# Performance work log

Measured on AMD Instinct MI355X. Metric: run time of the kernel, lower is better.

Reference implementation:

```python
import jax, jax.numpy as jnp
import numpy as np

B, S, D_MODEL, N_HEADS = 4, 8192, 1024, 16
D_K = D_MODEL // N_HEADS


def setup_inputs() -> dict:
    key = jax.random.key(0)
    k1, k2, k3 = jax.random.split(key, 3)
    x = jax.random.normal(k1, (B, S, D_MODEL), dtype=jnp.float32)
    w_qkv = jax.random.normal(k2, (D_MODEL, 3 * D_MODEL), dtype=jnp.float32) * (1.0 / np.sqrt(D_MODEL))
    w_o = jax.random.normal(k3, (D_MODEL, D_MODEL), dtype=jnp.float32) * (1.0 / np.sqrt(D_MODEL))
    return {"x": x, "w_qkv": w_qkv, "w_o": w_o}


def reference(x, w_qkv, w_o):
    b, s, dm = x.shape
    h, d = N_HEADS, D_K
    qkv = (x @ w_qkv).reshape(b, s, 3, h, d)  # (b, s, 3, h, d)
    q, k, v = qkv[:, :, 0], qkv[:, :, 1], qkv[:, :, 2]  # each (b, s, h, d)
    # ELU+1 feature map (positive features)
    q = jax.nn.elu(q) + 1.0
    k = jax.nn.elu(k) + 1.0
    # Global (non-causal) KV aggregation: (b, h, d, d)
    kv = jnp.einsum('bnhd,bnhf->bhdf', k, v)
    k_sum = k.sum(axis=1)  # (b, h, d)
    numerator = jnp.einsum('bnhd,bhdf->bnhf', q, kv)  # (b, s, h, d)
    denominator = jnp.einsum('bnhd,bhd->bnh', q, k_sum)[..., None] + 1e-6
    attn = (numerator / denominator).reshape(b, s, dm)
    return attn @ w_o
```

## Files before the change

kernel.cpp:

```cpp
#include <hip/hip_runtime.h>
#include <cmath>

constexpr int BB = 4;
constexpr int SS = 8192;
constexpr int DMODEL = 1024;
constexpr int NHEADS = 16;
constexpr int DHEAD = 64;
constexpr int MTOK = BB * SS;

typedef __attribute__((ext_vector_type(8))) short short8;
typedef __attribute__((ext_vector_type(4))) float f32x4;

__device__ __forceinline__ unsigned short f2bf(float f) {
    unsigned u = __float_as_uint(f);
    u += 0x7FFF + ((u >> 16) & 1);
    return (unsigned short)(u >> 16);
}
__device__ __forceinline__ float bf2f(unsigned short h) {
    return __uint_as_float(((unsigned)h) << 16);
}

__device__ __forceinline__ void stage_tile64(const unsigned short* g0, int ld,
                                             unsigned short* lds, int wave, int lane) {
#pragma unroll
    for (int i = 0; i < 4; ++i) {
        const int c = (wave * 4 + i) * 64 + lane;
        const int r = c >> 3;
        const int qg = (c & 7) ^ (r & 7);
        const unsigned short* g = g0 + (size_t)r * ld + qg * 8;
        unsigned short* l = lds + (wave * 4 + i) * 512;
        __builtin_amdgcn_global_load_lds(
            (const __attribute__((address_space(1))) unsigned int*)g,
            (__attribute__((address_space(3))) unsigned int*)l, 16, 0, 0);
    }
}

__device__ __forceinline__ short8 frag_ld64(const unsigned short* lds, int r, int q) {
    const int qs = q ^ (r & 7);
    return *(const short8*)(lds + r * 64 + qs * 8);
}

template <int EPI>
__global__ __launch_bounds__(256) void la_gemm(
    const unsigned short* __restrict__ A, const unsigned short* __restrict__ B,
    float* __restrict__ Cf,
    unsigned short* __restrict__ Cq, unsigned short* __restrict__ Ck,
    unsigned short* __restrict__ Cv,
    int N, int K)
{
    __shared__ __align__(16) unsigned short smem[2 * 8192];
    unsigned short* sA = smem;
    unsigned short* sB = smem + 8192;

    const int t = threadIdx.x;
    const int wave = t >> 6, lane = t & 63;
    const int wm = wave & 1, wn = wave >> 1;
    const int quad = lane >> 4, fl = lane & 15;
    const int m0 = blockIdx.y * 128, n0 = blockIdx.x * 128;

    const unsigned short* a_g = A + (size_t)m0 * K;
    const unsigned short* b_g = B + (size_t)n0 * K;

    f32x4 acc[4][4];
#pragma unroll
    for (int i = 0; i < 4; ++i)
#pragma unroll
        for (int j = 0; j < 4; ++j) acc[i][j] = (f32x4){0.f, 0.f, 0.f, 0.f};

    for (int kt = 0; kt < K; kt += 64) {
        __syncthreads();
        stage_tile64(a_g + kt, K, sA, wave, lane);
        stage_tile64(b_g + kt, K, sB, wave, lane);
        __syncthreads();

        short8 ah[4][2], bh[4][2];
#pragma unroll
        for (int i = 0; i < 4; ++i) {
            const int ra = wm * 64 + i * 16 + fl;
            const int rb = wn * 64 + i * 16 + fl;
#pragma unroll
            for (int s = 0; s < 2; ++s) {
                ah[i][s] = frag_ld64(sA, ra, s * 4 + quad);
                bh[i][s] = frag_ld64(sB, rb, s * 4 + quad);
            }
        }
#pragma unroll
        for (int s = 0; s < 2; ++s)
#pragma unroll
            for (int i = 0; i < 4; ++i)
#pragma unroll
                for (int j = 0; j < 4; ++j)
                    acc[i][j] = __builtin_amdgcn_mfma_f32_16x16x32_bf16(
                        ah[i][s], bh[j][s], acc[i][j], 0, 0, 0);
    }

    if (EPI == 1) {
        const int bsel = n0 >> 10;
        unsigned short* Cp = (bsel == 0) ? Cq : ((bsel == 1) ? Ck : Cv);
        const bool act = (bsel < 2);
        const int colb = (n0 & 1023) + wn * 64 + fl;
#pragma unroll
        for (int i = 0; i < 4; ++i) {
            const int rowb = m0 + wm * 64 + i * 16 + quad * 4;
#pragma unroll
            for (int j = 0; j < 4; ++j) {
                const int col = colb + j * 16;
#pragma unroll
                for (int r = 0; r < 4; ++r) {
                    float v = acc[i][j][r];
                    if (act) v = (v > 0.f) ? v + 1.f : __expf(v);
                    Cp[(size_t)(rowb + r) * 1024 + col] = f2bf(v);
                }
            }
        }
    } else {
#pragma unroll
        for (int i = 0; i < 4; ++i) {
            const int rowb = m0 + wm * 64 + i * 16 + quad * 4;
#pragma unroll
            for (int j = 0; j < 4; ++j) {
                const int col = n0 + wn * 64 + fl + j * 16;
#pragma unroll
                for (int r = 0; r < 4; ++r)
                    Cf[(size_t)(rowb + r) * N + col] = acc[i][j][r];
            }
        }
    }
}

__global__ __launch_bounds__(256) void cast_bf16(
    const float4* __restrict__ in, ushort4* __restrict__ hi, int n4)
{
    int i = blockIdx.x * 256 + threadIdx.x;
    const int stride = gridDim.x * 256;
    for (; i < n4; i += stride) {
        const float4 v = in[i];
        ushort4 h;
        h.x = f2bf(v.x); h.y = f2bf(v.y); h.z = f2bf(v.z); h.w = f2bf(v.w);
        hi[i] = h;
    }
}

__global__ __launch_bounds__(256) void cast_T(
    const float* __restrict__ w, unsigned short* __restrict__ hiT, int Kd, int Nd)
{
    __shared__ float tile[32][33];
    const int t = threadIdx.x;
    const int n0 = blockIdx.x * 32, k0 = blockIdx.y * 32;
    const int r = t >> 3, c4 = (t & 7) * 4;
    const float4 v = *(const float4*)(w + (size_t)(k0 + r) * Nd + n0 + c4);
    tile[r][c4 + 0] = v.x; tile[r][c4 + 1] = v.y;
    tile[r][c4 + 2] = v.z; tile[r][c4 + 3] = v.w;
    __syncthreads();
    ushort4 h;
    h.x = f2bf(tile[c4 + 0][r]); h.y = f2bf(tile[c4 + 1][r]);
    h.z = f2bf(tile[c4 + 2][r]); h.w = f2bf(tile[c4 + 3][r]);
    *(ushort4*)(hiT + (size_t)(n0 + r) * Kd + k0 + c4) = h;
}

constexpr int KV_CHUNKS = 16;

__global__ __launch_bounds__(256) void la_kvsum(
    const unsigned short* __restrict__ Kb, const unsigned short* __restrict__ Vb,
    float* __restrict__ kv, float* __restrict__ ksum)
{
    __shared__ float kk[32][68];
    __shared__ float vv[32][68];
    const int t = threadIdx.x;
    const int bh = blockIdx.x;
    const int b = bh >> 4, h = bh & 15;
    const int r = t >> 3, c8 = (t & 7) * 8;
    const int d0 = (t & 15) * 4, f0 = (t >> 4) * 4;
    float acc[4][4];
#pragma unroll
    for (int i = 0; i < 4; ++i)
#pragma unroll
        for (int j = 0; j < 4; ++j) acc[i][j] = 0.f;
    float ks = 0.f;
    const int s0 = blockIdx.y * (SS / KV_CHUNKS);

    for (int st = 0; st < SS / KV_CHUNKS; st += 32) {
        const size_t row = (size_t)(b * SS + s0 + st + r) * DMODEL + h * DHEAD + c8;
        const uint4 ku = *(const uint4*)(Kb + row);
        const uint4 vu = *(const uint4*)(Vb + row);
        __syncthreads();
        const unsigned ka_[4] = {ku.x, ku.y, ku.z, ku.w};
        const unsigned va_[4] = {vu.x, vu.y, vu.z, vu.w};
#pragma unroll
        for (int e = 0; e < 4; ++e) {
            kk[r][c8 + 2 * e]     = __uint_as_float(ka_[e] << 16);
            kk[r][c8 + 2 * e + 1] = __uint_as_float(ka_[e] & 0xFFFF0000u);
            vv[r][c8 + 2 * e]     = __uint_as_float(va_[e] << 16);
            vv[r][c8 + 2 * e + 1] = __uint_as_float(va_[e] & 0xFFFF0000u);
        }
        __syncthreads();
#pragma unroll 8
        for (int rr = 0; rr < 32; ++rr) {
            float4 kr = *(const float4*)&kk[rr][d0];
            float4 vr = *(const float4*)&vv[rr][f0];
            float ka[4] = {kr.x, kr.y, kr.z, kr.w};
            float va[4] = {vr.x, vr.y, vr.z, vr.w};
#pragma unroll
            for (int i = 0; i < 4; ++i)
#pragma unroll
                for (int j = 0; j < 4; ++j)
                    acc[i][j] = fmaf(ka[i], va[j], acc[i][j]);
        }
        if (t < 64) {
#pragma unroll 8
            for (int rr = 0; rr < 32; ++rr) ks += kk[rr][t];
        }
    }

    float* kvp = kv + (size_t)bh * DHEAD * DHEAD;
#pragma unroll
    for (int i = 0; i < 4; ++i)
#pragma unroll
        for (int j = 0; j < 4; ++j)
            atomicAdd(&kvp[(d0 + i) * DHEAD + f0 + j], acc[i][j]);
    if (t < 64) atomicAdd(&ksum[bh * DHEAD + t], ks);
}

__global__ __launch_bounds__(256) void la_attn(
    const unsigned short* __restrict__ Q, const float* __restrict__ kv,
    const float* __restrict__ ksum, unsigned short* __restrict__ attn)
{
    __shared__ float kvs[64][68];
    __shared__ float qs[64][68];
    __shared__ float kss[64];
    const int t = threadIdx.x;
    const int t0 = blockIdx.x * 64;
    const int b = t0 / SS;
    const int tok_g = t >> 4;
    const int f_g = t & 15;

    for (int hh = 0; hh < NHEADS; ++hh) {
        __syncthreads();
        const float* kvp = kv + (size_t)(b * NHEADS + hh) * DHEAD * DHEAD;
#pragma unroll
        for (int i = 0; i < 4; ++i) {
            const int idx = i * 256 + t;
            const int r = idx >> 4, c4 = (idx & 15) * 4;
            *(float4*)&kvs[r][c4] = *(const float4*)(kvp + r * 64 + c4);
        }
        if (t < 64) kss[t] = ksum[(b * NHEADS + hh) * DHEAD + t];
#pragma unroll
        for (int i = 0; i < 2; ++i) {
            const int idx = i * 256 + t;
            const int r = idx >> 3, c8 = (idx & 7) * 8;
            const uint4 qu = *(const uint4*)(Q + (size_t)(t0 + r) * DMODEL + hh * 64 + c8);
            const unsigned a[4] = {qu.x, qu.y, qu.z, qu.w};
#pragma unroll
            for (int e = 0; e < 4; ++e) {
                qs[r][c8 + 2 * e]     = __uint_as_float(a[e] << 16);
                qs[r][c8 + 2 * e + 1] = __uint_as_float(a[e] & 0xFFFF0000u);
            }
        }
        __syncthreads();

        float acc[4][4];
        float den[4];
#pragma unroll
        for (int i = 0; i < 4; ++i) {
            den[i] = 0.f;
#pragma unroll
            for (int j = 0; j < 4; ++j) acc[i][j] = 0.f;
        }
#pragma unroll 8
        for (int d = 0; d < 64; ++d) {
            const float4 kvf = *(const float4*)&kvs[d][f_g * 4];
            const float ks = kss[d];
#pragma unroll
            for (int i = 0; i < 4; ++i) {
                const float qd = qs[tok_g * 4 + i][d];
                den[i]    = fmaf(qd, ks,    den[i]);
                acc[i][0] = fmaf(qd, kvf.x, acc[i][0]);
                acc[i][1] = fmaf(qd, kvf.y, acc[i][1]);
                acc[i][2] = fmaf(qd, kvf.z, acc[i][2]);
                acc[i][3] = fmaf(qd, kvf.w, acc[i][3]);
            }
        }
#pragma unroll
        for (int i = 0; i < 4; ++i) {
            const float rcp = 1.f / (den[i] + 1e-6f);
            ushort4 o;
            o.x = f2bf(acc[i][0] * rcp); o.y = f2bf(acc[i][1] * rcp);
            o.z = f2bf(acc[i][2] * rcp); o.w = f2bf(acc[i][3] * rcp);
            *(ushort4*)(attn + (size_t)(t0 + tok_g * 4 + i) * DMODEL + hh * 64 + f_g * 4) = o;
        }
    }
}

__global__ void la_sentinel(float* out, int n) {
    int i = blockIdx.x * 256 + threadIdx.x;
    if (i < n) out[i] = 12345.0f;
}

extern "C" void kernel_launch(void* const* d_in, const int* in_sizes, int n_in,
                              void* d_out, int out_size, void* d_ws, size_t ws_size,
                              hipStream_t stream)
{
    const float* x     = (const float*)d_in[0];
    const float* w_qkv = (const float*)d_in[1];
    const float* w_o   = (const float*)d_in[2];
    float* out = (float*)d_out;

    char* p = (char*)d_ws;
    const size_t x_bf = (size_t)MTOK * DMODEL * 2;
    unsigned short* x_hi = (unsigned short*)p; p += x_bf;
    unsigned short* wqT = (unsigned short*)p; p += (size_t)3 * DMODEL * DMODEL * 2;
    unsigned short* woT = (unsigned short*)p; p += (size_t)DMODEL * DMODEL * 2;
    unsigned short* q_buf = (unsigned short*)p; p += x_bf;
    unsigned short* k_buf = (unsigned short*)p; p += x_bf;
    unsigned short* v_buf = (unsigned short*)p; p += x_bf;
    float* kvb = (float*)p; p += (size_t)BB * NHEADS * DHEAD * DHEAD * 4;
    float* ksb = (float*)p; p += (size_t)BB * NHEADS * DHEAD * 4;

    if ((size_t)(p - (char*)d_ws) > ws_size) {
        la_sentinel<<<(MTOK * DMODEL + 255) / 256, 256, 0, stream>>>(out, MTOK * DMODEL);
        return;
    }

    hipMemsetAsync(kvb, 0,
                   (size_t)(BB * NHEADS * DHEAD * DHEAD + BB * NHEADS * DHEAD) * sizeof(float),
                   stream);

    cast_bf16<<<8192, 256, 0, stream>>>((const float4*)x, (ushort4*)x_hi,
                                        MTOK * DMODEL / 4);
    cast_T<<<dim3(3 * DMODEL / 32, DMODEL / 32), 256, 0, stream>>>(w_qkv, wqT,
                                                                   DMODEL, 3 * DMODEL);
    cast_T<<<dim3(DMODEL / 32, DMODEL / 32), 256, 0, stream>>>(w_o, woT,
                                                               DMODEL, DMODEL);

    la_gemm<1><<<dim3(3 * DMODEL / 128, MTOK / 128), 256, 0, stream>>>(
        x_hi, wqT, nullptr, q_buf, k_buf, v_buf, 3 * DMODEL, DMODEL);

    la_kvsum<<<dim3(BB * NHEADS, KV_CHUNKS), 256, 0, stream>>>(k_buf, v_buf, kvb, ksb);

    la_attn<<<MTOK / 64, 256, 0, stream>>>(q_buf, kvb, ksb, x_hi);

    la_gemm<0><<<dim3(DMODEL / 128, MTOK / 128), 256, 0, stream>>>(
        x_hi, woT, out, nullptr, nullptr, nullptr, DMODEL, DMODEL);
}
```

Baseline: 829.1 us.

## Replace GEMM with 256x256 double-buffered pipelined kernel and XCD-aware tile remap

Replaces the 128x128 single-buffered bf16 MFMA GEMM with a 256x256-tile, 512-thread kernel. It double-buffers the K tiles in 128KB of dynamic LDS, interleaves global-to-LDS prefetch with MFMA phases, and uses barriers, waitcnt and setprio to keep the matrix units busy. Block ids are remapped so neighbouring tiles land on the same XCD, which should improve L2 reuse. The goal is to cut the load stalls and per-iteration syncs of the old GEMMs. In exchange, the larger tiles raise register pressure and lower occupancy, and the hand-placed waitcnt counts make the code fragile.

After: 723.6 us. 1.15x faster.

```diff
diff --git a/kernel.cpp b/kernel.cpp
--- a/kernel.cpp
+++ b/kernel.cpp
@@ -16,82 +16,172 @@
     u += 0x7FFF + ((u >> 16) & 1);
     return (unsigned short)(u >> 16);
 }
-__device__ __forceinline__ float bf2f(unsigned short h) {
-    return __uint_as_float(((unsigned)h) << 16);
-}
-
-__device__ __forceinline__ void stage_tile64(const unsigned short* g0, int ld,
-                                             unsigned short* lds, int wave, int lane) {
-#pragma unroll
-    for (int i = 0; i < 4; ++i) {
-        const int c = (wave * 4 + i) * 64 + lane;
-        const int r = c >> 3;
-        const int qg = (c & 7) ^ (r & 7);
-        const unsigned short* g = g0 + (size_t)r * ld + qg * 8;
-        unsigned short* l = lds + (wave * 4 + i) * 512;
-        __builtin_amdgcn_global_load_lds(
-            (const __attribute__((address_space(1))) unsigned int*)g,
-            (__attribute__((address_space(3))) unsigned int*)l, 16, 0, 0);
-    }
-}
-
-__device__ __forceinline__ short8 frag_ld64(const unsigned short* lds, int r, int q) {
-    const int qs = q ^ (r & 7);
-    return *(const short8*)(lds + r * 64 + qs * 8);
-}
+
+#define STAGE2(gbase, lbase)                                                          \
+    do {                                                                              \
+        __builtin_amdgcn_global_load_lds(                                             \
+            (const __attribute__((address_space(1))) unsigned int*)((gbase) + o0),    \
+            (__attribute__((address_space(3))) unsigned int*)((lbase) + d0), 16, 0, 0);\
+        __builtin_amdgcn_global_load_lds(                                             \
+            (const __attribute__((address_space(1))) unsigned int*)((gbase) + o1),    \
+            (__attribute__((address_space(3))) unsigned int*)((lbase) + d1), 16, 0, 0);\
+    } while (0)
 
 template <int EPI>
-__global__ __launch_bounds__(256) void la_gemm(
+__global__ __launch_bounds__(512, 2) void la_gemm256(
     const unsigned short* __restrict__ A, const unsigned short* __restrict__ B,
     float* __restrict__ Cf,
     unsigned short* __restrict__ Cq, unsigned short* __restrict__ Ck,
     unsigned short* __restrict__ Cv,
-    int N, int K)
-{
-    __shared__ __align__(16) unsigned short smem[2 * 8192];
-    unsigned short* sA = smem;
-    unsigned short* sB = smem + 8192;
+    const int N, const int K, const int GX)
+{
+    extern __shared__ __align__(16) unsigned short smem[];
 
     const int t = threadIdx.x;
     const int wave = t >> 6, lane = t & 63;
-    const int wm = wave & 1, wn = wave >> 1;
+    const int wm = wave >> 2, wn = wave & 3;
     const int quad = lane >> 4, fl = lane & 15;
-    const int m0 = blockIdx.y * 128, n0 = blockIdx.x * 128;
+
+    const int nwg = (int)gridDim.x;
+    const int cpx = nwg >> 3;
+    const int id = ((int)blockIdx.x & 7) * cpx + ((int)blockIdx.x >> 3);
+    const int bx = id % GX, by = id / GX;
+    const int m0 = by * 256, n0 = bx * 256;
 
     const unsigned short* a_g = A + (size_t)m0 * K;
     const unsigned short* b_g = B + (size_t)n0 * K;
 
-    f32x4 acc[4][4];
-#pragma unroll
-    for (int i = 0; i < 4; ++i)
+    const int c0 = t, c1 = 512 + t;
+    const size_t o0 = (size_t)(c0 >> 2) * K + (size_t)((((c0 & 3) ^ ((c0 >> 2) & 3))) << 3);
+    const size_t o1 = (size_t)(c1 >> 2) * K + (size_t)((((c1 & 3) ^ ((c1 >> 2) & 3))) << 3);
+    const int d0 = c0 * 8, d1 = c1 * 8;
+
+    const int qsc = (quad ^ (fl & 3)) << 3;
+    const int offA = (wm * 128 + fl) * 32 + qsc;
+    const int offB = (wn * 64 + fl) * 32 + qsc;
+
+    f32x4 acc[8][4];
+#pragma unroll
+    for (int i = 0; i < 8; ++i)
 #pragma unroll
         for (int j = 0; j < 4; ++j) acc[i][j] = (f32x4){0.f, 0.f, 0.f, 0.f};
 
-    for (int kt = 0; kt < K; kt += 64) {
-        __syncthreads();
-        stage_tile64(a_g + kt, K, sA, wave, lane);
-        stage_tile64(b_g + kt, K, sB, wave, lane);
-        __syncthreads();
-
-        short8 ah[4][2], bh[4][2];
-#pragma unroll
-        for (int i = 0; i < 4; ++i) {
-            const int ra = wm * 64 + i * 16 + fl;
-            const int rb = wn * 64 + i * 16 + fl;
-#pragma unroll
-            for (int s = 0; s < 2; ++s) {
-                ah[i][s] = frag_ld64(sA, ra, s * 4 + quad);
-                bh[i][s] = frag_ld64(sB, rb, s * 4 + quad);
-            }
-        }
-#pragma unroll
-        for (int s = 0; s < 2; ++s)
-#pragma unroll
-            for (int i = 0; i < 4; ++i)
-#pragma unroll
-                for (int j = 0; j < 4; ++j)
-                    acc[i][j] = __builtin_amdgcn_mfma_f32_16x16x32_bf16(
-                        ah[i][s], bh[j][s], acc[i][j], 0, 0, 0);
+    unsigned short* bufc = smem;
+    unsigned short* bufn = smem + 32768;
+
+    STAGE2(a_g,      bufc);
+    STAGE2(b_g,      bufc + 16384);
+    STAGE2(a_g + 32, bufc + 8192);
+    STAGE2(b_g + 32, bufc + 24576);
+    asm volatile("s_waitcnt vmcnt(4)" ::: "memory");
+    __builtin_amdgcn_s_barrier();
+
+    for (int kt = 0; kt < K - 64; kt += 64) {
+        const unsigned short* an = a_g + kt + 64;
+        const unsigned short* bn = b_g + kt + 64;
+        short8 ah[4], bh[4];
+
+#pragma unroll
+        for (int i = 0; i < 4; ++i) ah[i] = *(const short8*)(bufc + offA + i * 512);
+#pragma unroll
+        for (int j = 0; j < 4; ++j) bh[j] = *(const short8*)(bufc + 16384 + offB + j * 512);
+        STAGE2(an, bufn);
+        __builtin_amdgcn_s_barrier();
+        asm volatile("s_waitcnt lgkmcnt(0)" ::: "memory");
+        __builtin_amdgcn_s_setprio(1);
+#pragma unroll
+        for (int i = 0; i < 4; ++i)
+#pragma unroll
+            for (int j = 0; j < 4; ++j)
+                acc[i][j] = __builtin_amdgcn_mfma_f32_16x16x32_bf16(ah[i], bh[j], acc[i][j], 0, 0, 0);
+        __builtin_amdgcn_s_setprio(0);
+        __builtin_amdgcn_s_barrier();
+
+#pragma unroll
+        for (int i = 0; i < 4; ++i) ah[i] = *(const short8*)(bufc + offA + 2048 + i * 512);
+        STAGE2(bn, bufn + 16384);
+        __builtin_amdgcn_s_barrier();
+        asm volatile("s_waitcnt lgkmcnt(0)" ::: "memory");
+        __builtin_amdgcn_s_setprio(1);
+#pragma unroll
+        for (int i = 0; i < 4; ++i)
+#pragma unroll
+            for (int j = 0; j < 4; ++j)
+                acc[4 + i][j] = __builtin_amdgcn_mfma_f32_16x16x32_bf16(ah[i], bh[j], acc[4 + i][j], 0, 0, 0);
+        __builtin_amdgcn_s_setprio(0);
+        asm volatile("s_waitcnt vmcnt(4)" ::: "memory");
+        __builtin_amdgcn_s_barrier();
+
+#pragma unroll
+        for (int i = 0; i < 4; ++i) ah[i] = *(const short8*)(bufc + 8192 + offA + i * 512);
+#pragma unroll
+        for (int j = 0; j < 4; ++j) bh[j] = *(const short8*)(bufc + 24576 + offB + j * 512);
+        STAGE2(an + 32, bufn + 8192);
+        __builtin_amdgcn_s_barrier();
+        asm volatile("s_waitcnt lgkmcnt(0)" ::: "memory");
+        __builtin_amdgcn_s_setprio(1);
+#pragma unroll
+        for (int i = 0; i < 4; ++i)
+#pragma unroll
+            for (int j = 0; j < 4; ++j)
+                acc[i][j] = __builtin_amdgcn_mfma_f32_16x16x32_bf16(ah[i], bh[j], acc[i][j], 0, 0, 0);
+        __builtin_amdgcn_s_setprio(0);
+        __builtin_amdgcn_s_barrier();
+
+#pragma unroll
+        for (int i = 0; i < 4; ++i) ah[i] = *(const short8*)(bufc + 8192 + offA + 2048 + i * 512);
+        STAGE2(bn + 32, bufn + 24576);
+        __builtin_amdgcn_s_barrier();
+        asm volatile("s_waitcnt lgkmcnt(0)" ::: "memory");
+        __builtin_amdgcn_s_setprio(1);
+#pragma unroll
+        for (int i = 0; i < 4; ++i)
+#pragma unroll
+            for (int j = 0; j < 4; ++j)
+                acc[4 + i][j] = __builtin_amdgcn_mfma_f32_16x16x32_bf16(ah[i], bh[j], acc[4 + i][j], 0, 0, 0);
+        __builtin_amdgcn_s_setprio(0);
+        asm volatile("s_waitcnt vmcnt(4)" ::: "memory");
+        __builtin_amdgcn_s_barrier();
+
+        unsigned short* tmp = bufc; bufc = bufn; bufn = tmp;
+    }
+
+    {
+        short8 ah[4], bh[4];
+#pragma unroll
+        for (int i = 0; i < 4; ++i) ah[i] = *(const short8*)(bufc + offA + i * 512);
+#pragma unroll
+        for (int j = 0; j < 4; ++j) bh[j] = *(const short8*)(bufc + 16384 + offB + j * 512);
+#pragma unroll
+        for (int i = 0; i < 4; ++i)
+#pragma unroll
+            for (int j = 0; j < 4; ++j)
+                acc[i][j] = __builtin_amdgcn_mfma_f32_16x16x32_bf16(ah[i], bh[j], acc[i][j], 0, 0, 0);
+#pragma unroll
+        for (int i = 0; i < 4; ++i) ah[i] = *(const short8*)(bufc + offA + 2048 + i * 512);
+#pragma unroll
+        for (int i = 0; i < 4; ++i)
+#pragma unroll
+            for (int j = 0; j < 4; ++j)
+                acc[4 + i][j] = __builtin_amdgcn_mfma_f32_16x16x32_bf16(ah[i], bh[j], acc[4 + i][j], 0, 0, 0);
+        asm volatile("s_waitcnt vmcnt(0)" ::: "memory");
+        __builtin_amdgcn_s_barrier();
+#pragma unroll
+        for (int i = 0; i < 4; ++i) ah[i] = *(const short8*)(bufc + 8192 + offA + i * 512);
+#pragma unroll
+        for (int j = 0; j < 4; ++j) bh[j] = *(const short8*)(bufc + 24576 + offB + j * 512);
+#pragma unroll
+        for (int i = 0; i < 4; ++i)
+#pragma unroll
+            for (int j = 0; j < 4; ++j)
+                acc[i][j] = __builtin_amdgcn_mfma_f32_16x16x32_bf16(ah[i], bh[j], acc[i][j], 0, 0, 0);
+#pragma unroll
+        for (int i = 0; i < 4; ++i) ah[i] = *(const short8*)(bufc + 8192 + offA + 2048 + i * 512);
+#pragma unroll
+        for (int i = 0; i < 4; ++i)
+#pragma unroll
+            for (int j = 0; j < 4; ++j)
+                acc[4 + i][j] = __builtin_amdgcn_mfma_f32_16x16x32_bf16(ah[i], bh[j], acc[4 + i][j], 0, 0, 0);
     }
 
     if (EPI == 1) {
@@ -100,8 +190,8 @@
         const bool act = (bsel < 2);
         const int colb = (n0 & 1023) + wn * 64 + fl;
 #pragma unroll
-        for (int i = 0; i < 4; ++i) {
-            const int rowb = m0 + wm * 64 + i * 16 + quad * 4;
+        for (int i = 0; i < 8; ++i) {
+            const int rowb = m0 + wm * 128 + i * 16 + quad * 4;
 #pragma unroll
             for (int j = 0; j < 4; ++j) {
                 const int col = colb + j * 16;
@@ -115,8 +205,8 @@
         }
     } else {
 #pragma unroll
-        for (int i = 0; i < 4; ++i) {
-            const int rowb = m0 + wm * 64 + i * 16 + quad * 4;
+        for (int i = 0; i < 8; ++i) {
+            const int rowb = m0 + wm * 128 + i * 16 + quad * 4;
 #pragma unroll
             for (int j = 0; j < 4; ++j) {
                 const int col = n0 + wn * 64 + fl + j * 16;
@@ -305,6 +395,15 @@
     const float* w_o   = (const float*)d_in[2];
     float* out = (float*)d_out;
 
+    static bool attr_done = []() {
+        hipFuncSetAttribute((const void*)&la_gemm256<1>,
+                            hipFuncAttributeMaxDynamicSharedMemorySize, 131072);
+        hipFuncSetAttribute((const void*)&la_gemm256<0>,
+                            hipFuncAttributeMaxDynamicSharedMemorySize, 131072);
+        return true;
+    }();
+    (void)attr_done;
+
     char* p = (char*)d_ws;
     const size_t x_bf = (size_t)MTOK * DMODEL * 2;
     unsigned short* x_hi = (unsigned short*)p; p += x_bf;
@@ -332,13 +431,13 @@
     cast_T<<<dim3(DMODEL / 32, DMODEL / 32), 256, 0, stream>>>(w_o, woT,
                                                                DMODEL, DMODEL);
 
-    la_gemm<1><<<dim3(3 * DMODEL / 128, MTOK / 128), 256, 0, stream>>>(
-        x_hi, wqT, nullptr, q_buf, k_buf, v_buf, 3 * DMODEL, DMODEL);
+    la_gemm256<1><<<(3 * DMODEL / 256) * (MTOK / 256), 512, 131072, stream>>>(
+        x_hi, wqT, nullptr, q_buf, k_buf, v_buf, 3 * DMODEL, DMODEL, 3 * DMODEL / 256);
 
     la_kvsum<<<dim3(BB * NHEADS, KV_CHUNKS), 256, 0, stream>>>(k_buf, v_buf, kvb, ksb);
 
     la_attn<<<MTOK / 64, 256, 0, stream>>>(q_buf, kvb, ksb, x_hi);
 
-    la_gemm<0><<<dim3(DMODEL / 128, MTOK / 128), 256, 0, stream>>>(
-        x_hi, woT, out, nullptr, nullptr, nullptr, DMODEL, DMODEL);
-}
+    la_gemm256<0><<<(DMODEL / 256) * (MTOK / 256), 512, 131072, stream>>>(
+        x_hi, woT, out, nullptr, nullptr, nullptr, DMODEL, DMODEL, DMODEL / 256);
+}
```
